# Performance work log

Measured on AMD Instinct MI355X. Metric: run time of the kernel, lower is better.

The kernel has to match this reference:

```python
import jax, jax.numpy as jnp
import numpy as np

B, NV, C = 4, 32768, 128
NCLS, K = 10, 500
GRID = 180  # spatial extent at feature_map_stride=8 (1440/8)
STRIDE = 8.0
PCR = np.array([-54.0, -54.0, -5.0, 54.0, 54.0, 3.0], np.float32)
VOX = np.array([0.075, 0.075, 0.2], np.float32)
LIMIT = np.array([-61.2, -61.2, -10.0, 61.2, 61.2, 10.0], np.float32)
SCORE_THRESH = 0.1
BN_EPS = 1e-5


def setup_inputs() -> dict:
    key = jax.random.key(0)
    ks = jax.random.split(key, 24)
    s = 1.0 / np.sqrt(C)
    inp = {}
    inp['feats'] = jax.random.normal(ks[0], (B * NV, C), jnp.float32)
    inp['voxel_xy'] = jax.random.randint(ks[1], (B * NV, 2), 0, GRID, dtype=jnp.int32)
    inp['W1'] = jax.random.normal(ks[2], (6, C, C), jnp.float32) * s
    inp['b1'] = jax.random.normal(ks[3], (6, C), jnp.float32) * 0.01
    inp['bn_gamma'] = 1.0 + 0.1 * jax.random.normal(ks[4], (6, C), jnp.float32)
    inp['bn_beta'] = 0.1 * jax.random.normal(ks[5], (6, C), jnp.float32)
    inp['bn_mean'] = 0.1 * jax.random.normal(ks[6], (6, C), jnp.float32)
    inp['bn_var'] = 0.5 + jax.random.uniform(ks[7], (6, C), jnp.float32)
    outs = [('hm', NCLS), ('center', 2), ('center_z', 1), ('dim', 3), ('rot', 2), ('vel', 2)]
    for i, (name, oc) in enumerate(outs):
        sc = 0.05 if name == 'dim' else s  # keep dim.exp() in a sane range
        inp['W2_' + name] = jax.random.normal(ks[8 + 2 * i], (C, oc), jnp.float32) * sc
        inp['b2_' + name] = jax.random.normal(ks[9 + 2 * i], (oc,), jnp.float32) * 0.01
    inp['batch_size'] = B
    return inp


def _forward(feats, voxel_xy, W1, b1, bn_gamma, bn_beta, bn_mean, bn_var,
             W2_hm, b2_hm, W2_center, b2_center, W2_center_z, b2_center_z,
             W2_dim, b2_dim, W2_rot, b2_rot, W2_vel, b2_vel, batch_size):
    Bs = batch_size
    N = feats.shape[0]
    Nv = N // Bs
    # --- separate heads: SubMConv2d(k=1)==per-voxel linear; BN in eval mode ---
    h = jnp.einsum('nc,bcd->bnd', feats, W1) + b1[:, None, :]            # [6,N,C]
    inv = bn_gamma / jnp.sqrt(bn_var + BN_EPS)
    h = jax.nn.relu((h - bn_mean[:, None, :]) * inv[:, None, :] + bn_beta[:, None, :])
    hm = jax.nn.sigmoid(h[0] @ W2_hm + b2_hm)                            # [N,NCLS]
    center = h[1] @ W2_center + b2_center                                # [N,2]
    center_z = h[2] @ W2_center_z + b2_center_z                          # [N,1]
    dim = jnp.exp(h[3] @ W2_dim + b2_dim)                                # [N,3]
    rot = h[4] @ W2_rot + b2_rot                                         # [N,2] (cos,sin)
    vel = h[5] @ W2_vel + b2_vel                                         # [N,2]
    # --- CenterNet-style decode (nuscenes _topk_1d): per-class topk then global topk ---
    hm_b = hm.reshape(Bs, Nv, NCLS)
    sc_c, idx_c = jax.lax.top_k(jnp.transpose(hm_b, (0, 2, 1)), K)       # [B,NCLS,K]
    topk_score, topk_ind = jax.lax.top_k(sc_c.reshape(Bs, NCLS * K), K)  # [B,K]
    class_ids = topk_ind // K                                            # [B,K]
    vox_ind = jnp.take_along_axis(idx_c.reshape(Bs, NCLS * K), topk_ind, axis=1)  # [B,K] in [0,Nv)

    def gather(x):  # x: [N,d] -> [B,K,d]
        return jnp.take_along_axis(x.reshape(Bs, Nv, -1), vox_ind[:, :, None], axis=1)

    ctr = gather(center)
    cz = gather(center_z)
    dm = gather(dim)
    rt = gather(rot)
    vl = gather(vel)
    xy = gather(voxel_xy.astype(jnp.float32))
    angle = jnp.arctan2(rt[..., 1:2], rt[..., 0:1])
    xs = (xy[..., 0:1] + ctr[..., 0:1]) * STRIDE * VOX[0] + PCR[0]
    ys = (xy[..., 1:2] + ctr[..., 1:2]) * STRIDE * VOX[1] + PCR[1]
    boxes = jnp.concatenate([xs, ys, cz, dm, angle, vl], axis=-1)        # [B,K,9]
    lim = jnp.asarray(LIMIT)
    mask = (jnp.all(boxes[..., :3] >= lim[:3], axis=-1)
            & jnp.all(boxes[..., :3] <= lim[3:], axis=-1)
            & (topk_score > SCORE_THRESH))                               # [B,K]
    boxes_scores = jnp.concatenate([boxes, topk_score[..., None]], -1) * mask[..., None].astype(boxes.dtype)
    labels = jnp.where(mask, class_ids + 1, 0)                           # class_id_mapping identity, +1
    voxel_ids = vox_ind + (jnp.arange(Bs, dtype=vox_ind.dtype) * Nv)[:, None]  # global add_features ids
    return boxes_scores, labels, voxel_ids, mask


def reference(feats, voxel_xy, W1, b1, bn_gamma, bn_beta, bn_mean, bn_var,
              W2_hm, b2_hm, W2_center, b2_center, W2_center_z, b2_center_z,
              W2_dim, b2_dim, W2_rot, b2_rot, W2_vel, b2_vel, batch_size):
    return _forward(feats, voxel_xy, W1, b1, bn_gamma, bn_beta, bn_mean, bn_var,
                    W2_hm, b2_hm, W2_center, b2_center, W2_center_z, b2_center_z,
                    W2_dim, b2_dim, W2_rot, b2_rot, W2_vel, b2_vel, batch_size)
```

## Files before the change

kernel.cpp:

```cpp
#include <hip/hip_runtime.h>
#include <math.h>

#define NV 32768
#define CD 128
#define NCLS 10
#define KSEL 500
#define BNEPS 1e-5f
#define NK (NCLS * NV)
#define H20CUT 0x3E000
#define H20BINS 6144
#define CANDCAP 2048
#define NCHUNK 64
#define CHUNKV (NK / NCHUNK)
#define CHUNK4 (CHUNKV / 4)

__global__ __launch_bounds__(256, 4) void stageA_kernel(
    const float* __restrict__ feats,
    const float* __restrict__ W1,
    const float* __restrict__ b1,
    const float* __restrict__ bng,
    const float* __restrict__ bnb,
    const float* __restrict__ bnm,
    const float* __restrict__ bnv,
    const float* __restrict__ W2hm,
    const float* __restrict__ b2hm,
    unsigned int* __restrict__ scoreb,
    unsigned int* __restrict__ zbase,
    int zwords)
{
    __shared__ __align__(16) float smem[64 * 129];
    __shared__ float w2s[CD * NCLS];
    __shared__ float b2s[NCLS];
    float4* const fsmv = (float4*)smem;

    const int tid = threadIdx.x;
    const int gbase = blockIdx.x * 64;

    if (blockIdx.x == 0) {
        for (int i = tid; i < zwords; i += 256) zbase[i] = 0u;
    }

    for (int i = tid; i < CD * NCLS; i += 256) w2s[i] = W2hm[i];
    if (tid < NCLS) b2s[tid] = b2hm[tid];

    for (int t = tid; t < 64 * 32; t += 256) {
        const int r = t >> 5;
        const int g = t & 31;
        const float4 v = *(const float4*)(feats + (((size_t)(gbase + r)) << 7) + (g << 2));
        fsmv[r * 32 + (g ^ (r & 31))] = v;
    }
    __syncthreads();

    const int c0 = (tid & 15) << 3;
    const int r0 = (tid >> 4) << 2;

    float acc[4][8];
    #pragma unroll
    for (int i = 0; i < 4; ++i)
        #pragma unroll
        for (int j = 0; j < 8; ++j) acc[i][j] = 0.f;

    #pragma unroll 2
    for (int kc = 0; kc < 32; ++kc) {
        float4 fr[4];
        #pragma unroll
        for (int i = 0; i < 4; ++i) {
            const int row = r0 + i;
            fr[i] = fsmv[row * 32 + (kc ^ (row & 31))];
        }
        const float* frp = (const float*)&fr[0];
        #pragma unroll
        for (int kk = 0; kk < 4; ++kk) {
            const int k = (kc << 2) + kk;
            const float4 wa = *(const float4*)(W1 + (k << 7) + c0);
            const float4 wb = *(const float4*)(W1 + (k << 7) + c0 + 4);
            const float w[8] = {wa.x, wa.y, wa.z, wa.w, wb.x, wb.y, wb.z, wb.w};
            #pragma unroll
            for (int ri = 0; ri < 4; ++ri) {
                const float f = frp[ri * 4 + kk];
                #pragma unroll
                for (int ci = 0; ci < 8; ++ci)
                    acc[ri][ci] = fmaf(f, w[ci], acc[ri][ci]);
            }
        }
    }
    __syncthreads();

    #pragma unroll
    for (int ci = 0; ci < 8; ++ci) {
        const int c = c0 + ci;
        const float inv = bng[c] / sqrtf(bnv[c] + BNEPS);
        const float mu = bnm[c];
        const float be = bnb[c];
        const float bb = b1[c];
        #pragma unroll
        for (int ri = 0; ri < 4; ++ri) {
            const float h = (acc[ri][ci] + bb - mu) * inv + be;
            acc[ri][ci] = fmaxf(h, 0.f);
        }
    }
    #pragma unroll
    for (int ri = 0; ri < 4; ++ri)
        #pragma unroll
        for (int ci = 0; ci < 8; ++ci)
            smem[(r0 + ri) * 129 + c0 + ci] = acc[ri][ci];
    __syncthreads();

    const int r = tid & 63;
    const int ogrp = tid >> 6;
    float lg[3] = {0.f, 0.f, 0.f};
    for (int c = 0; c < 128; ++c) {
        const float a = smem[r * 129 + c];
        #pragma unroll
        for (int i = 0; i < 3; ++i) {
            const int o = ogrp + 4 * i;
            if (o < NCLS) lg[i] = fmaf(a, w2s[c * NCLS + o], lg[i]);
        }
    }
    const int n = gbase + r;
    const int b = n >> 15;
    const int v = n & (NV - 1);
    unsigned int* sb = scoreb + (size_t)b * NK;
    #pragma unroll
    for (int i = 0; i < 3; ++i) {
        const int o = ogrp + 4 * i;
        if (o < NCLS) {
            const float x = lg[i] + b2s[o];
            const float s = 1.f / (1.f + expf(-x));
            sb[o * NV + v] = __float_as_uint(s);
        }
    }
}

__global__ __launch_bounds__(256) void stageB1_kernel(
    const unsigned int* __restrict__ scoreb,
    unsigned int* __restrict__ hist20)
{
    __shared__ unsigned int lh[H20BINS];
    const int tid = threadIdx.x;
    const int b = blockIdx.y;
    const uint4* sb4 = (const uint4*)(scoreb + (size_t)b * NK) + (size_t)blockIdx.x * CHUNK4;

    for (int i = tid; i < H20BINS; i += 256) lh[i] = 0u;
    __syncthreads();

    #pragma unroll
    for (int q = 0; q < 5; ++q) {
        const uint4 v = sb4[q * 256 + tid];
        const unsigned int sv[4] = {v.x, v.y, v.z, v.w};
        #pragma unroll
        for (int k = 0; k < 4; ++k) {
            const int rel = (int)(sv[k] >> 12) - H20CUT;
            if (rel >= 0) atomicAdd(&lh[rel], 1u);
        }
    }
    __syncthreads();

    unsigned int* gh = hist20 + (size_t)b * H20BINS;
    for (int i = tid; i < H20BINS; i += 256) {
        const unsigned int v = lh[i];
        if (v) atomicAdd(&gh[i], v);
    }
}

__global__ __launch_bounds__(256) void stageB2_kernel(
    const unsigned int* __restrict__ scoreb,
    const unsigned int* __restrict__ hist20,
    unsigned int* __restrict__ cnt,
    unsigned long long* __restrict__ cand)
{
    __shared__ unsigned int hh[H20BINS];
    __shared__ unsigned int part[256];
    __shared__ unsigned int sT;
    const int tid = threadIdx.x;
    const int b = blockIdx.y;

    const unsigned int* gh = hist20 + (size_t)b * H20BINS;
    for (int i = tid; i < H20BINS; i += 256) hh[i] = gh[i];
    __syncthreads();

    unsigned int Ls = 0;
    #pragma unroll
    for (int i = 0; i < 24; ++i) Ls += hh[tid * 24 + i];
    part[tid] = Ls;
    __syncthreads();

    for (int off = 1; off < 256; off <<= 1) {
        const unsigned int add = (tid + off < 256) ? part[tid + off] : 0u;
        __syncthreads();
        part[tid] += add;
        __syncthreads();
    }
    const unsigned int incl = part[tid];
    const unsigned int above_seg = incl - Ls;

    if (above_seg < KSEL && incl >= KSEL) {
        int above = (int)above_seg;
        int tbin = tid * 24;
        for (int i = 23; i >= 0; --i) {
            const int c = (int)hh[tid * 24 + i];
            if (above + c >= KSEL) { tbin = tid * 24 + i; break; }
            above += c;
        }
        sT = ((unsigned int)(tbin + H20CUT)) << 12;
    }
    if (tid == 0 && incl < KSEL) sT = ((unsigned int)H20CUT) << 12;
    __syncthreads();
    const unsigned int T = sT;

    const uint4* sb4 = (const uint4*)(scoreb + (size_t)b * NK) + (size_t)blockIdx.x * CHUNK4;
    #pragma unroll
    for (int q = 0; q < 5; ++q) {
        const int vi = q * 256 + tid;
        const uint4 v = sb4[vi];
        const unsigned int sv[4] = {v.x, v.y, v.z, v.w};
        const unsigned int i0 = (unsigned int)((blockIdx.x * CHUNK4 + vi) * 4);
        #pragma unroll
        for (int k = 0; k < 4; ++k) {
            if (sv[k] >= T) {
                const unsigned int p = atomicAdd(&cnt[b], 1u);
                if (p < CANDCAP)
                    cand[(size_t)b * CANDCAP + p] =
                        ((unsigned long long)sv[k] << 32) |
                        (unsigned long long)(0xFFFFFFFFu - (i0 + k));
            }
        }
    }
}

__global__ __launch_bounds__(1024) void stageB3_kernel(
    const unsigned long long* __restrict__ cand,
    const unsigned int* __restrict__ cnt,
    float* __restrict__ sel_score,
    int* __restrict__ sel_cls,
    int* __restrict__ sel_vox)
{
    __shared__ unsigned long long kbuf[CANDCAP];
    const int b = blockIdx.x;
    const int tid = threadIdx.x;
    const int n = min((int)cnt[b], CANDCAP);
    int m = 512;
    while (m < n) m <<= 1;
    for (int i = tid; i < m; i += 1024)
        kbuf[i] = (i < n) ? cand[(size_t)b * CANDCAP + i] : 0ull;
    __syncthreads();
    for (int size = 2; size <= m; size <<= 1) {
        for (int stride = size >> 1; stride > 0; stride >>= 1) {
            for (int j = tid; j < m; j += 1024) {
                const int p = j ^ stride;
                if (p > j) {
                    const unsigned long long x = kbuf[j];
                    const unsigned long long y = kbuf[p];
                    const bool descRegion = ((j & size) == 0);
                    if ((x < y) == descRegion) { kbuf[j] = y; kbuf[p] = x; }
                }
            }
            __syncthreads();
        }
    }
    if (tid < KSEL) {
        const unsigned long long kk = kbuf[tid];
        const unsigned int s32 = (unsigned int)(kk >> 32);
        const unsigned int fl = 0xFFFFFFFFu - (unsigned int)(kk & 0xFFFFFFFFull);
        const int idx = b * KSEL + tid;
        sel_score[idx] = __uint_as_float(s32);
        sel_cls[idx] = (int)(fl >> 15);
        sel_vox[idx] = (int)(fl & (NV - 1));
    }
}

__global__ __launch_bounds__(256) void stageCD_kernel(
    const float* __restrict__ feats,
    const int* __restrict__ voxel_xy,
    const float* __restrict__ sel_score,
    const int* __restrict__ sel_cls,
    const int* __restrict__ sel_vox,
    const float* __restrict__ W1,
    const float* __restrict__ b1,
    const float* __restrict__ bng,
    const float* __restrict__ bnb,
    const float* __restrict__ bnm,
    const float* __restrict__ bnv,
    const float* __restrict__ W2c, const float* __restrict__ b2c,
    const float* __restrict__ W2z, const float* __restrict__ b2z,
    const float* __restrict__ W2d, const float* __restrict__ b2d,
    const float* __restrict__ W2r, const float* __restrict__ b2r,
    const float* __restrict__ W2v, const float* __restrict__ b2v,
    float* __restrict__ out,
    int total)
{
    __shared__ float fs[4][128];
    __shared__ float as_[4][128];
    __shared__ float dec_s[4][10];
    __shared__ int vsel[4];
    const int tid = threadIdx.x;
    const int s0 = blockIdx.x * 4;

    if (tid < 4) {
        const int s = s0 + tid;
        vsel[tid] = (s / KSEL) * NV + sel_vox[s];
    }
    __syncthreads();
    for (int t = tid; t < 4 * 128; t += 256) {
        const int j = t >> 7;
        const int c = t & 127;
        fs[j][c] = feats[((size_t)vsel[j] << 7) + c];
    }
    __syncthreads();

    const int c = tid & 127;
    const int jh = tid >> 7;

    for (int head = 1; head <= 5; ++head) {
        float acc[2] = {0.f, 0.f};
        const float* Wh = W1 + head * (CD * CD);
        for (int k = 0; k < 128; ++k) {
            const float w = Wh[(k << 7) + c];
            #pragma unroll
            for (int jj = 0; jj < 2; ++jj)
                acc[jj] = fmaf(fs[jh * 2 + jj][k], w, acc[jj]);
        }
        const int hc = head * CD + c;
        const float inv = bng[hc] / sqrtf(bnv[hc] + BNEPS);
        const float mu = bnm[hc], be = bnb[hc], bb = b1[hc];
        #pragma unroll
        for (int jj = 0; jj < 2; ++jj) {
            const float h = (acc[jj] + bb - mu) * inv + be;
            as_[jh * 2 + jj][c] = fmaxf(h, 0.f);
        }
        __syncthreads();

        const float* w2; const float* bb2; int oc, off; bool ex = false;
        if (head == 1)      { w2 = W2c; bb2 = b2c; oc = 2; off = 0; }
        else if (head == 2) { w2 = W2z; bb2 = b2z; oc = 1; off = 2; }
        else if (head == 3) { w2 = W2d; bb2 = b2d; oc = 3; off = 3; ex = true; }
        else if (head == 4) { w2 = W2r; bb2 = b2r; oc = 2; off = 6; }
        else                { w2 = W2v; bb2 = b2v; oc = 2; off = 8; }

        if (tid < 4 * oc) {
            const int j = tid / oc;
            const int o = tid % oc;
            float a = 0.f;
            for (int cc = 0; cc < 128; ++cc) a = fmaf(as_[j][cc], w2[cc * oc + o], a);
            a += bb2[o];
            if (ex) a = expf(a);
            dec_s[j][off + o] = a;
        }
        __syncthreads();
    }

    if (tid < 4) {
        const int s = s0 + tid;
        const int b = s / KSEL;
        const float score = sel_score[s];
        const int cls = sel_cls[s];
        const int v = sel_vox[s];
        const int n = b * NV + v;
        const float xi = (float)voxel_xy[2 * n];
        const float yi = (float)voxel_xy[2 * n + 1];
        const float* dd = dec_s[tid];
        const float cx = dd[0], cy = dd[1], cz = dd[2];
        const float d0 = dd[3], d1 = dd[4], d2 = dd[5];
        const float rc = dd[6], rs = dd[7], ve0 = dd[8], ve1 = dd[9];
        const float SV = 0.075f * 8.0f;
        const float xs = (xi + cx) * SV + (-54.0f);
        const float ys = (yi + cy) * SV + (-54.0f);
        const float ang = atan2f(rs, rc);
        const bool mk = (xs >= -61.2f) && (ys >= -61.2f) && (cz >= -10.0f) &&
                        (xs <= 61.2f) && (ys <= 61.2f) && (cz <= 10.0f) &&
                        (score > 0.1f);
        const float m = mk ? 1.f : 0.f;
        float* bx = out + (size_t)s * 10;
        bx[0] = xs * m; bx[1] = ys * m; bx[2] = cz * m;
        bx[3] = d0 * m; bx[4] = d1 * m; bx[5] = d2 * m;
        bx[6] = ang * m; bx[7] = ve0 * m; bx[8] = ve1 * m; bx[9] = score * m;
        out[(size_t)total * 10 + s] = mk ? (float)(cls + 1) : 0.f;
        out[(size_t)total * 11 + s] = (float)n;
        out[(size_t)total * 12 + s] = m;
    }
}

extern "C" void kernel_launch(void* const* d_in, const int* in_sizes, int n_in,
                              void* d_out, int out_size, void* d_ws, size_t ws_size,
                              hipStream_t stream) {
    const float* feats   = (const float*)d_in[0];
    const int*   voxelxy = (const int*)d_in[1];
    const float* W1   = (const float*)d_in[2];
    const float* b1   = (const float*)d_in[3];
    const float* bng  = (const float*)d_in[4];
    const float* bnb  = (const float*)d_in[5];
    const float* bnm  = (const float*)d_in[6];
    const float* bnv  = (const float*)d_in[7];
    const float* W2hm = (const float*)d_in[8];
    const float* b2hm = (const float*)d_in[9];
    const float* W2c  = (const float*)d_in[10];
    const float* b2c  = (const float*)d_in[11];
    const float* W2z  = (const float*)d_in[12];
    const float* b2z  = (const float*)d_in[13];
    const float* W2d  = (const float*)d_in[14];
    const float* b2d  = (const float*)d_in[15];
    const float* W2r  = (const float*)d_in[16];
    const float* b2r  = (const float*)d_in[17];
    const float* W2v  = (const float*)d_in[18];
    const float* b2v  = (const float*)d_in[19];

    const int B = in_sizes[0] / (NV * CD);
    const int N = B * NV;
    const int total = B * KSEL;

    char* ws = (char*)d_ws;
    unsigned int* scoreb = (unsigned int*)ws;            ws += (size_t)B * NK * 4;
    unsigned int* hist20 = (unsigned int*)ws;            ws += (size_t)B * H20BINS * 4;
    unsigned int* cnt    = (unsigned int*)ws;            ws += 8 * 4;
    unsigned long long* cand = (unsigned long long*)ws;  ws += (size_t)B * CANDCAP * 8;
    float* sel_score = (float*)ws;                       ws += (size_t)total * 4;
    int*   sel_cls   = (int*)ws;                         ws += (size_t)total * 4;
    int*   sel_vox   = (int*)ws;                         ws += (size_t)total * 4;

    const int zwords = B * H20BINS + 8;

    stageA_kernel<<<dim3(N / 64), dim3(256), 0, stream>>>(
        feats, W1, b1, bng, bnb, bnm, bnv, W2hm, b2hm, scoreb, hist20, zwords);

    stageB1_kernel<<<dim3(NCHUNK, B), dim3(256), 0, stream>>>(scoreb, hist20);
    stageB2_kernel<<<dim3(NCHUNK, B), dim3(256), 0, stream>>>(scoreb, hist20, cnt, cand);
    stageB3_kernel<<<dim3(B), dim3(1024), 0, stream>>>(
        cand, cnt, sel_score, sel_cls, sel_vox);

    stageCD_kernel<<<dim3(total / 4), dim3(256), 0, stream>>>(
        feats, voxelxy, sel_score, sel_cls, sel_vox,
        W1, b1, bng, bnb, bnm, bnv,
        W2c, b2c, W2z, b2z, W2d, b2d, W2r, b2r, W2v, b2v,
        (float*)d_out, total);
}
```

Baseline: 304.6 us.

## Double-buffer stage A operand loads and parallelize stage CD heads across threads

In stage A, the GEMM inner loop now uses explicit double buffering: the next k-chunk's feature and weight registers are loaded while the current chunk is computed, to hide load latency. The occupancy hint drops from 4 to 3 blocks per SM to leave room for the extra registers. Stage CD launches 640 threads so all five heads run at once, each thread handling all four selected voxels. This removes the per-head serial loop and its barriers, and the 40 second-layer dot products run in a single pass. The risks are higher register pressure and lower occupancy in stage A, and more idle threads in stage CD.

```diff
diff --git a/kernel.cpp b/kernel.cpp
--- a/kernel.cpp
+++ b/kernel.cpp
@@ -14,7 +14,7 @@
 #define CHUNKV (NK / NCHUNK)
 #define CHUNK4 (CHUNKV / 4)
 
-__global__ __launch_bounds__(256, 4) void stageA_kernel(
+__global__ __launch_bounds__(256, 3) void stageA_kernel(
     const float* __restrict__ feats,
     const float* __restrict__ W1,
     const float* __restrict__ b1,
@@ -53,6 +53,7 @@
 
     const int c0 = (tid & 15) << 3;
     const int r0 = (tid >> 4) << 2;
+    const float* const Wc0 = W1 + c0;
 
     float acc[4][8];
     #pragma unroll
@@ -60,30 +61,59 @@
         #pragma unroll
         for (int j = 0; j < 8; ++j) acc[i][j] = 0.f;
 
-    #pragma unroll 2
-    for (int kc = 0; kc < 32; ++kc) {
-        float4 fr[4];
-        #pragma unroll
-        for (int i = 0; i < 4; ++i) {
-            const int row = r0 + i;
-            fr[i] = fsmv[row * 32 + (kc ^ (row & 31))];
-        }
-        const float* frp = (const float*)&fr[0];
-        #pragma unroll
-        for (int kk = 0; kk < 4; ++kk) {
-            const int k = (kc << 2) + kk;
-            const float4 wa = *(const float4*)(W1 + (k << 7) + c0);
-            const float4 wb = *(const float4*)(W1 + (k << 7) + c0 + 4);
-            const float w[8] = {wa.x, wa.y, wa.z, wa.w, wb.x, wb.y, wb.z, wb.w};
-            #pragma unroll
-            for (int ri = 0; ri < 4; ++ri) {
-                const float f = frp[ri * 4 + kk];
-                #pragma unroll
-                for (int ci = 0; ci < 8; ++ci)
-                    acc[ri][ci] = fmaf(f, w[ci], acc[ri][ci]);
-            }
-        }
-    }
+    float4 frA[4], frB[4], wA[8], wB[8];
+
+    #pragma unroll
+    for (int i = 0; i < 4; ++i) {
+        const int row = r0 + i;
+        frA[i] = fsmv[row * 32 + (0 ^ (row & 31))];
+    }
+    #pragma unroll
+    for (int kk = 0; kk < 4; ++kk) {
+        wA[2 * kk]     = *(const float4*)(Wc0 + (kk << 7));
+        wA[2 * kk + 1] = *(const float4*)(Wc0 + (kk << 7) + 4);
+    }
+
+#define SA_PREFETCH(FR, WW, KC)                                           \
+    {                                                                     \
+        const int kc_ = (KC);                                             \
+        _Pragma("unroll")                                                 \
+        for (int i = 0; i < 4; ++i) {                                     \
+            const int row = r0 + i;                                       \
+            FR[i] = fsmv[row * 32 + (kc_ ^ (row & 31))];                  \
+        }                                                                 \
+        const int kb_ = kc_ << 2;                                         \
+        _Pragma("unroll")                                                 \
+        for (int kk = 0; kk < 4; ++kk) {                                  \
+            WW[2 * kk]     = *(const float4*)(Wc0 + ((kb_ + kk) << 7));   \
+            WW[2 * kk + 1] = *(const float4*)(Wc0 + ((kb_ + kk) << 7) + 4); \
+        }                                                                 \
+    }
+
+#define SA_COMPUTE(FR, WW)                                                \
+    {                                                                     \
+        const float* frp = (const float*)FR;                              \
+        const float* wp  = (const float*)WW;                              \
+        _Pragma("unroll")                                                 \
+        for (int kk = 0; kk < 4; ++kk)                                    \
+            _Pragma("unroll")                                             \
+            for (int ri = 0; ri < 4; ++ri) {                              \
+                const float f = frp[ri * 4 + kk];                         \
+                _Pragma("unroll")                                         \
+                for (int ci = 0; ci < 8; ++ci)                            \
+                    acc[ri][ci] = fmaf(f, wp[kk * 8 + ci], acc[ri][ci]);  \
+            }                                                             \
+    }
+
+    for (int kc = 0; kc < 32; kc += 2) {
+        SA_PREFETCH(frB, wB, kc + 1)
+        SA_COMPUTE(frA, wA)
+        SA_PREFETCH(frA, wA, (kc + 2) & 31)
+        SA_COMPUTE(frB, wB)
+    }
+#undef SA_PREFETCH
+#undef SA_COMPUTE
+
     __syncthreads();
 
     #pragma unroll
@@ -269,7 +299,7 @@
     }
 }
 
-__global__ __launch_bounds__(256) void stageCD_kernel(
+__global__ __launch_bounds__(640) void stageCD_kernel(
     const float* __restrict__ feats,
     const int* __restrict__ voxel_xy,
     const float* __restrict__ sel_score,
@@ -290,7 +320,7 @@
     int total)
 {
     __shared__ float fs[4][128];
-    __shared__ float as_[4][128];
+    __shared__ float as_[5][4][128];
     __shared__ float dec_s[4][10];
     __shared__ int vsel[4];
     const int tid = threadIdx.x;
@@ -301,53 +331,53 @@
         vsel[tid] = (s / KSEL) * NV + sel_vox[s];
     }
     __syncthreads();
-    for (int t = tid; t < 4 * 128; t += 256) {
-        const int j = t >> 7;
-        const int c = t & 127;
+    if (tid < 512) {
+        const int j = tid >> 7;
+        const int c = tid & 127;
         fs[j][c] = feats[((size_t)vsel[j] << 7) + c];
     }
     __syncthreads();
 
-    const int c = tid & 127;
-    const int jh = tid >> 7;
-
-    for (int head = 1; head <= 5; ++head) {
-        float acc[2] = {0.f, 0.f};
-        const float* Wh = W1 + head * (CD * CD);
+    {
+        const int h = tid / 128;
+        const int c = tid & 127;
+        const int head = h + 1;
+        float acc[4] = {0.f, 0.f, 0.f, 0.f};
+        const float* Wh = W1 + head * (CD * CD) + c;
         for (int k = 0; k < 128; ++k) {
-            const float w = Wh[(k << 7) + c];
+            const float w = Wh[k << 7];
             #pragma unroll
-            for (int jj = 0; jj < 2; ++jj)
-                acc[jj] = fmaf(fs[jh * 2 + jj][k], w, acc[jj]);
+            for (int j = 0; j < 4; ++j)
+                acc[j] = fmaf(fs[j][k], w, acc[j]);
         }
         const int hc = head * CD + c;
         const float inv = bng[hc] / sqrtf(bnv[hc] + BNEPS);
         const float mu = bnm[hc], be = bnb[hc], bb = b1[hc];
         #pragma unroll
-        for (int jj = 0; jj < 2; ++jj) {
-            const float h = (acc[jj] + bb - mu) * inv + be;
-            as_[jh * 2 + jj][c] = fmaxf(h, 0.f);
-        }
-        __syncthreads();
-
-        const float* w2; const float* bb2; int oc, off; bool ex = false;
-        if (head == 1)      { w2 = W2c; bb2 = b2c; oc = 2; off = 0; }
-        else if (head == 2) { w2 = W2z; bb2 = b2z; oc = 1; off = 2; }
-        else if (head == 3) { w2 = W2d; bb2 = b2d; oc = 3; off = 3; ex = true; }
-        else if (head == 4) { w2 = W2r; bb2 = b2r; oc = 2; off = 6; }
-        else                { w2 = W2v; bb2 = b2v; oc = 2; off = 8; }
-
-        if (tid < 4 * oc) {
-            const int j = tid / oc;
-            const int o = tid % oc;
-            float a = 0.f;
-            for (int cc = 0; cc < 128; ++cc) a = fmaf(as_[j][cc], w2[cc * oc + o], a);
-            a += bb2[o];
-            if (ex) a = expf(a);
-            dec_s[j][off + o] = a;
-        }
-        __syncthreads();
-    }
+        for (int j = 0; j < 4; ++j) {
+            const float hv = (acc[j] + bb - mu) * inv + be;
+            as_[h][j][c] = fmaxf(hv, 0.f);
+        }
+    }
+    __syncthreads();
+
+    if (tid < 40) {
+        const int j = tid / 10;
+        const int slot = tid % 10;
+        const float* w2; const float* bb2; int hh, o, oc; bool ex = false;
+        if (slot < 2)      { w2 = W2c; bb2 = b2c; hh = 0; o = slot;     oc = 2; }
+        else if (slot < 3) { w2 = W2z; bb2 = b2z; hh = 1; o = 0;        oc = 1; }
+        else if (slot < 6) { w2 = W2d; bb2 = b2d; hh = 2; o = slot - 3; oc = 3; ex = true; }
+        else if (slot < 8) { w2 = W2r; bb2 = b2r; hh = 3; o = slot - 6; oc = 2; }
+        else               { w2 = W2v; bb2 = b2v; hh = 4; o = slot - 8; oc = 2; }
+        float a = 0.f;
+        for (int cc = 0; cc < 128; ++cc)
+            a = fmaf(as_[hh][j][cc], w2[cc * oc + o], a);
+        a += bb2[o];
+        if (ex) a = expf(a);
+        dec_s[j][slot] = a;
+    }
+    __syncthreads();
 
     if (tid < 4) {
         const int s = s0 + tid;
@@ -427,7 +457,7 @@
     stageB3_kernel<<<dim3(B), dim3(1024), 0, stream>>>(
         cand, cnt, sel_score, sel_cls, sel_vox);
 
-    stageCD_kernel<<<dim3(total / 4), dim3(256), 0, stream>>>(
+    stageCD_kernel<<<dim3(total / 4), dim3(640), 0, stream>>>(
         feats, voxelxy, sel_score, sel_cls, sel_vox,
         W1, b1, bng, bnb, bnm, bnv,
         W2c, b2c, W2z, b2z, W2d, b2d, W2r, b2r, W2v, b2v,
```

After: 274.3 us. 1.11x faster.
